# Optimization experiments

Measured on AMD Instinct MI355X. Metric: run time of the kernel, lower is better.

## Reference

```python
import jax, jax.numpy as jnp
import numpy as np

B, T, N, D = 16, 32, 1024, 64
H = 64            # gru_hidden_size
HEADS = 4
GH = 128          # gat_hidden_size (heads concatenated)
F = GH // HEADS   # per-head dim = 32
R = 128           # res_hidden_size
O = 32            # output_size


def setup_inputs() -> dict:
    key = jax.random.key(0)
    ks = jax.random.split(key, 26)
    rn = lambda k, s, sc=0.05: jax.random.normal(k, s, jnp.float32) * sc
    return {
        'sequential_inputs': jax.random.normal(ks[0], (B, T, N, D), jnp.float32),
        'adj_matrix': jax.random.randint(ks[1], (N, N), 0, 2, jnp.int32),
        'Wih0': rn(ks[2], (3 * H, D)), 'Whh0': rn(ks[3], (3 * H, H)),
        'bih0': rn(ks[4], (3 * H,)), 'bhh0': rn(ks[5], (3 * H,)),
        'Wih1': rn(ks[6], (3 * H, H)), 'Whh1': rn(ks[7], (3 * H, H)),
        'bih1': rn(ks[8], (3 * H,)), 'bhh1': rn(ks[9], (3 * H,)),
        'gatW': rn(ks[10], (H, HEADS, F)),
        'a_src': rn(ks[11], (HEADS, F)), 'a_dst': rn(ks[12], (HEADS, F)),
        'rW1': rn(ks[13], (GH, R)), 'rb1': rn(ks[14], (R,)),
        'rW2': rn(ks[15], (R, R)), 'rb2': rn(ks[16], (R,)),
        'fW': rn(ks[17], (R, O)), 'fb': rn(ks[18], (O,)),
        'ln_g': jnp.ones((O,), jnp.float32), 'ln_b': jnp.zeros((O,), jnp.float32),
        'nW1': rn(ks[19], (O, O)), 'nb1': rn(ks[20], (O,)),
        'nW2': rn(ks[21], (O, O)), 'nb2': rn(ks[22], (O,)),
    }


def gru_layer(x, Wih, Whh, bih, bhh):
    # x: [BN, T, Din] -> hidden states [BN, T, H] (PyTorch GRU cell math)
    bn = x.shape[0]
    hdim = Whh.shape[1]

    def step(h, x_t):
        gi = x_t @ Wih.T + bih
        gh = h @ Whh.T + bhh
        ir, iz, inn = jnp.split(gi, 3, axis=-1)
        hr, hz, hn = jnp.split(gh, 3, axis=-1)
        r = jax.nn.sigmoid(ir + hr)
        z = jax.nn.sigmoid(iz + hz)
        n = jnp.tanh(inn + r * hn)
        h_new = (1.0 - z) * n + z * h
        return h_new, h_new

    h0 = jnp.zeros((bn, hdim), x.dtype)
    _, hs = jax.lax.scan(step, h0, jnp.swapaxes(x, 0, 1))
    return jnp.swapaxes(hs, 0, 1)


def forward(seq, adj, Wih0, Whh0, bih0, bhh0, Wih1, Whh1, bih1, bhh1,
            gatW, a_src, a_dst, rW1, rb1, rW2, rb2, fW, fb, ln_g, ln_b,
            nW1, nb1, nW2, nb2):
    b, t, n, d = seq.shape
    # faithful to torch .view(B*N, T, D) on a [B,T,N,D] tensor: raw reshape
    x = seq.reshape(b * n, t, d)
    h1 = gru_layer(x, Wih0, Whh0, bih0, bhh0)
    h2 = gru_layer(h1, Wih1, Whh1, bih1, bhh1)
    gru_feat = h2[:, -1, :].reshape(b, n, -1)  # [B, N, H]

    # multi-head GAT, vectorized over batch (masked additive attention)
    Wh = jnp.einsum('bnd,dhf->bnhf', gru_feat, gatW)          # [B,N,HEADS,F]
    src = jnp.einsum('bnhf,hf->bnh', Wh, a_src)
    dst = jnp.einsum('bnhf,hf->bnh', Wh, a_dst)
    e = jax.nn.leaky_relu(src[:, :, None, :] + dst[:, None, :, :], 0.2)  # [B,N,N,HEADS]
    mask = (adj > 0)[None, :, :, None]
    e = jnp.where(mask, e, -1e9)
    attn = jax.nn.softmax(e, axis=2)                          # softmax over neighbors j
    gat = jnp.einsum('bijh,bjhf->bihf', attn, Wh).reshape(b, n, GH)
    gat = jax.nn.elu(gat)

    # Res-C: Linear-ReLU-Linear + identity skip, ReLU
    z = gat.reshape(b * n, GH)
    r = jax.nn.relu(z @ rW1 + rb1) @ rW2 + rb2
    res = jax.nn.relu(z + r)

    # Full-C: Linear -> LayerNorm -> tanh (dropout = identity in eval)
    y = res @ fW + fb
    mu = y.mean(-1, keepdims=True)
    var = ((y - mu) ** 2).mean(-1, keepdims=True)
    y = jnp.tanh((y - mu) * jax.lax.rsqrt(var + 1e-5) * ln_g + ln_b)

    # NN layer: Linear-ReLU-Linear
    out = (jax.nn.relu(y @ nW1 + nb1) @ nW2 + nb2).reshape(b, n, O)
    return out, attn


def reference(sequential_inputs, adj_matrix, Wih0, Whh0, bih0, bhh0, Wih1, Whh1,
              bih1, bhh1, gatW, a_src, a_dst, rW1, rb1, rW2, rb2, fW, fb,
              ln_g, ln_b, nW1, nb1, nW2, nb2):
    return forward(sequential_inputs, adj_matrix, Wih0, Whh0, bih0, bhh0,
                   Wih1, Whh1, bih1, bhh1, gatW, a_src, a_dst, rW1, rb1,
                   rW2, rb2, fW, fb, ln_g, ln_b, nW1, nb1, nW2, nb2)
```

## Files before the change

kernel.cpp:

```cpp
#include <hip/hip_runtime.h>

#define BB 16
#define TT 32
#define NN 1024
#define DD 64
#define HH 64
#define BN 16384
#define GH 128
#define RR 128
#define OO 32

#define LOG2E 1.44269504088896f

typedef __attribute__((ext_vector_type(8))) short short8;
typedef __attribute__((ext_vector_type(4))) float f32x4;
typedef __attribute__((ext_vector_type(8))) _Float16 half8;
typedef __attribute__((ext_vector_type(2))) __fp16 fp16x2;

#define MF16(A, B, C) __builtin_amdgcn_mfma_f32_16x16x32_f16((A), (B), (C), 0, 0, 0)

__device__ __forceinline__ float rcp_fast(float x) {
  return __builtin_amdgcn_rcpf(x);
}
__device__ __forceinline__ float exp2_fast(float x) {
  return __builtin_amdgcn_exp2f(x);
}
__device__ __forceinline__ float sigmoid2(float a) {
  return rcp_fast(1.0f + exp2_fast(-a));
}
__device__ __forceinline__ float tanh2(float a) {
  return fmaf(-2.0f, rcp_fast(exp2_fast(2.0f * a) + 1.0f), 1.0f);
}
__device__ __forceinline__ float tanh_e(float x) {
  return tanh2(x * LOG2E);
}
__device__ __forceinline__ float leaky02(float x) {
  return fmaxf(x, 0.2f * x);
}

__global__ __launch_bounds__(512, 4) void gru_fused_kernel(
    const float* __restrict__ x,
    const float* __restrict__ Wih0, const float* __restrict__ Whh0,
    const float* __restrict__ bih0, const float* __restrict__ bhh0,
    const float* __restrict__ Wih1, const float* __restrict__ Whh1,
    const float* __restrict__ bih1, const float* __restrict__ bhh1,
    const float* __restrict__ gatW, const float* __restrict__ a_src,
    const float* __restrict__ a_dst,
    float* __restrict__ Wh, float* __restrict__ srcv, float* __restrict__ dstv)
{
  __shared__ _Float16 sX[2][2048];
  __shared__ _Float16 sH0[2][2048];
  __shared__ _Float16 sH1[2][2048];

  const int tid = threadIdx.x;
  const int gbase = blockIdx.x * 32;

  const int w = tid >> 6, l = tid & 63;
  const int layer = w >> 2;
  const int jt = w & 3;
  const int c = l & 15;
  const int rq = l >> 4;

  const float* Wih = layer ? Wih1 : Wih0;
  const float* Whh = layer ? Whh1 : Whh0;
  const float* bihp = layer ? bih1 : bih0;
  const float* bhhp = layer ? bhh1 : bhh0;

  half8 wf[3][2][2];
#pragma unroll
  for (int g = 0; g < 3; ++g) {
    const int row = g * 64 + jt * 16 + c;
#pragma unroll
    for (int ks = 0; ks < 2; ++ks) {
      const int col = ks * 32 + (rq << 3);
      float4 i0 = *reinterpret_cast<const float4*>(Wih + row * 64 + col);
      float4 i1 = *reinterpret_cast<const float4*>(Wih + row * 64 + col + 4);
      float4 h0 = *reinterpret_cast<const float4*>(Whh + row * 64 + col);
      float4 h1 = *reinterpret_cast<const float4*>(Whh + row * 64 + col + 4);
      float wi[8] = {i0.x, i0.y, i0.z, i0.w, i1.x, i1.y, i1.z, i1.w};
      float wh[8] = {h0.x, h0.y, h0.z, h0.w, h1.x, h1.y, h1.z, h1.w};
      half8 vih, vhh;
#pragma unroll
      for (int e = 0; e < 8; ++e) {
        vih[e] = (_Float16)(wi[e] * LOG2E);
        vhh[e] = (_Float16)(wh[e] * LOG2E);
      }
      wf[g][0][ks] = vih;
      wf[g][1][ks] = vhh;
    }
  }

  const int sseq = tid >> 4;
  const int kq = (tid & 15) << 2;
  const float* xrow = x + (size_t)(gbase + sseq) * (TT * 64) + kq;
  const int sxoff = sseq * 64 + (kq ^ ((sseq & 7) << 3));

  for (int i = tid; i < 2048; i += 512) {
    sH0[0][i] = (_Float16)0.0f;
    sH1[0][i] = (_Float16)0.0f;
  }

  float4 p = *reinterpret_cast<const float4*>(xrow);
  *reinterpret_cast<fp16x2*>(&sX[0][sxoff])     = __builtin_amdgcn_cvt_pkrtz(p.x, p.y);
  *reinterpret_cast<fp16x2*>(&sX[0][sxoff + 2]) = __builtin_amdgcn_cvt_pkrtz(p.z, p.w);
  p = *reinterpret_cast<const float4*>(xrow + 64);

  const int jj = jt * 16 + c;
  const float br  = (bihp[jj]       + bhhp[jj])      * LOG2E;
  const float bz  = (bihp[64 + jj]  + bhhp[64 + jj]) * LOG2E;
  const float bni = bihp[128 + jj] * LOG2E;
  const float bnh = bhhp[128 + jj] * LOG2E;

  int ao[2][2];
#pragma unroll
  for (int mi = 0; mi < 2; ++mi)
#pragma unroll
    for (int ks = 0; ks < 2; ++ks)
      ao[mi][ks] = (mi * 16 + c) * 64 + (((ks << 5) + (rq << 3)) ^ ((c & 7) << 3));
  int hoff[2][4];
#pragma unroll
  for (int mi = 0; mi < 2; ++mi)
#pragma unroll
    for (int q = 0; q < 4; ++q) {
      const int seq = mi * 16 + (rq << 2) + q;
      hoff[mi][q] = seq * 64 + (jj ^ ((seq & 7) << 3));
    }

  float h[2][4];
#pragma unroll
  for (int mi = 0; mi < 2; ++mi)
#pragma unroll
    for (int q = 0; q < 4; ++q) h[mi][q] = 0.0f;

  for (int t = 0; t <= TT; ++t) {
    __syncthreads();
    const int cb = t & 1, nb = cb ^ 1;
    if (t + 1 < TT) {
      *reinterpret_cast<fp16x2*>(&sX[nb][sxoff])     = __builtin_amdgcn_cvt_pkrtz(p.x, p.y);
      *reinterpret_cast<fp16x2*>(&sX[nb][sxoff + 2]) = __builtin_amdgcn_cvt_pkrtz(p.z, p.w);
    }
    if (t + 2 < TT)
      p = *reinterpret_cast<const float4*>(xrow + (t + 2) * 64);

    const bool active = layer ? (t >= 1) : (t < TT);
    if (active) {
      const _Float16* xsrc = layer ? &sH0[cb][0] : &sX[cb][0];
      const _Float16* hsrc = layer ? &sH1[nb][0] : &sH0[cb][0];
      _Float16* hdst       = layer ? &sH1[cb][0] : &sH0[nb][0];

      f32x4 accr[2], accz[2], accni[2], accnh[2];
#pragma unroll
      for (int mi = 0; mi < 2; ++mi) {
        accr[mi]  = (f32x4){br, br, br, br};
        accz[mi]  = (f32x4){bz, bz, bz, bz};
        accni[mi] = (f32x4){bni, bni, bni, bni};
        accnh[mi] = (f32x4){bnh, bnh, bnh, bnh};
      }

#pragma unroll
      for (int ks = 0; ks < 2; ++ks) {
#pragma unroll
        for (int mi = 0; mi < 2; ++mi) {
          const half8 xa = *reinterpret_cast<const half8*>(xsrc + ao[mi][ks]);
          const half8 ha = *reinterpret_cast<const half8*>(hsrc + ao[mi][ks]);
          accr[mi]  = MF16(xa, wf[0][0][ks], accr[mi]);
          accr[mi]  = MF16(ha, wf[0][1][ks], accr[mi]);
          accz[mi]  = MF16(xa, wf[1][0][ks], accz[mi]);
          accz[mi]  = MF16(ha, wf[1][1][ks], accz[mi]);
          accni[mi] = MF16(xa, wf[2][0][ks], accni[mi]);
          accnh[mi] = MF16(ha, wf[2][1][ks], accnh[mi]);
        }
      }

#pragma unroll
      for (int mi = 0; mi < 2; ++mi)
#pragma unroll
        for (int q = 0; q < 4; ++q) {
          float rg = sigmoid2(accr[mi][q]);
          float zg = sigmoid2(accz[mi][q]);
          float ng = tanh2(fmaf(rg, accnh[mi][q], accni[mi][q]));
          float hv = fmaf(zg, h[mi][q] - ng, ng);
          h[mi][q] = hv;
          hdst[hoff[mi][q]] = (_Float16)hv;
        }
    }
  }

  __syncthreads();
  float* sRed = reinterpret_cast<float*>(&sX[0][0]);
  {
    const int col = (w << 4) + c;
    half8 gb[2];
#pragma unroll
    for (int ks = 0; ks < 2; ++ks)
#pragma unroll
      for (int e = 0; e < 8; ++e) {
        const int k = ks * 32 + (rq << 3) + e;
        gb[ks][e] = (_Float16)gatW[k * 128 + col];
      }
    const float as = a_src[col], ad = a_dst[col];
    f32x4 accw[2];
#pragma unroll
    for (int mi = 0; mi < 2; ++mi) {
      accw[mi] = (f32x4){0.f, 0.f, 0.f, 0.f};
#pragma unroll
      for (int ks = 0; ks < 2; ++ks) {
        const half8 fa = *reinterpret_cast<const half8*>(&sH1[0][0] + ao[mi][ks]);
        accw[mi] = MF16(fa, gb[ks], accw[mi]);
      }
    }
#pragma unroll
    for (int mi = 0; mi < 2; ++mi)
#pragma unroll
      for (int q = 0; q < 4; ++q) {
        const int seq = mi * 16 + (rq << 2) + q;
        Wh[(size_t)(gbase + seq) * 128 + col] = accw[mi][q];
        float s = accw[mi][q] * as, d = accw[mi][q] * ad;
#pragma unroll
        for (int mm = 1; mm < 16; mm <<= 1) {
          s += __shfl_xor(s, mm, 64);
          d += __shfl_xor(d, mm, 64);
        }
        if (c == 0) {
          sRed[w * 32 + seq]       = s;
          sRed[256 + w * 32 + seq] = d;
        }
      }
  }
  __syncthreads();
  if (tid < 256) {
    const int hh = tid >> 6;
    const int rem = tid & 63;
    const int sd = rem >> 5;
    const int ii = rem & 31;
    const float v = sRed[sd * 256 + (hh * 2) * 32 + ii] +
                    sRed[sd * 256 + (hh * 2 + 1) * 32 + ii];
    float* outp = sd ? dstv : srcv;
    outp[(size_t)(gbase + ii) * 4 + hh] = v;
  }
}

__global__ __launch_bounds__(256) void attn_kernel(
    const float* __restrict__ Wh, const float* __restrict__ srcp,
    const float* __restrict__ dstp, const int* __restrict__ adj,
    float* __restrict__ attn_out, float* __restrict__ gat_out)
{
  __shared__ __align__(16) float sDst[4096];
  __shared__ __align__(16) float sSrc[128];
  __shared__ __align__(16) float sIS[128];
  __shared__ unsigned int sAdjW[32][32];
  __shared__ __align__(16) _Float16 sP[2][4][32][40];
  __shared__ __align__(16) _Float16 sB[2][4][32][40];

  const int tid = threadIdx.x;
  const int bid = blockIdx.x;
  const int swzb = ((bid & 7) << 6) | (bid >> 3);
  const int b = swzb >> 5;
  const int itile = (swzb & 31) << 5;

  for (int idx = tid; idx < 4096; idx += 256)
    sDst[idx] = dstp[(size_t)b * 4096 + idx] * LOG2E;
  if (tid < 128)
    sSrc[tid] = srcp[((size_t)b * 1024 + itile) * 4 + tid] * LOG2E;

  {
    const int row = tid >> 3;
    const int w0 = (tid & 7) << 2;
    const int* arow_g = adj + (size_t)(itile + row) * 1024 + (w0 << 5);
#pragma unroll
    for (int wq = 0; wq < 4; ++wq) {
      unsigned int word = 0;
#pragma unroll
      for (int c4 = 0; c4 < 8; ++c4) {
        int4 v = *reinterpret_cast<const int4*>(arow_g + (wq << 5) + (c4 << 2));
        word |= (unsigned)((v.x != 0) ? 1 : 0) << (c4 * 4 + 0);
        word |= (unsigned)((v.y != 0) ? 1 : 0) << (c4 * 4 + 1);
        word |= (unsigned)((v.z != 0) ? 1 : 0) << (c4 * 4 + 2);
        word |= (unsigned)((v.w != 0) ? 1 : 0) << (c4 * 4 + 3);
      }
      sAdjW[row][w0 + wq] = word;
    }
  }
  __syncthreads();

  {
    const int i = tid >> 3;
    const int par = tid & 7;
    const float4 sv = *reinterpret_cast<const float4*>(&sSrc[i * 4]);
    f32x4 acc = (f32x4){0.f, 0.f, 0.f, 0.f};
    const unsigned int bit0 = 1u << par;
    for (int kw = 0; kw < 32; ++kw) {
      const unsigned int word = sAdjW[i][kw];
#pragma unroll
      for (int e = 0; e < 4; ++e) {
        const int gj = (kw << 5) + (e << 3) + par;
        const float4 dv = *reinterpret_cast<const float4*>(&sDst[gj * 4]);
        const float mf = (word & (bit0 << (e << 3))) ? 1.0f : 0.0f;
        acc[0] = fmaf(mf, exp2_fast(leaky02(sv.x + dv.x)), acc[0]);
        acc[1] = fmaf(mf, exp2_fast(leaky02(sv.y + dv.y)), acc[1]);
        acc[2] = fmaf(mf, exp2_fast(leaky02(sv.z + dv.z)), acc[2]);
        acc[3] = fmaf(mf, exp2_fast(leaky02(sv.w + dv.w)), acc[3]);
      }
    }
#pragma unroll
    for (int m = 1; m < 8; m <<= 1) {
#pragma unroll
      for (int q = 0; q < 4; ++q) acc[q] += __shfl_xor(acc[q], m, 64);
    }
    if (par == 0) {
      float4 isv;
      isv.x = acc[0] > 0.f ? rcp_fast(acc[0]) : -1.0f;
      isv.y = acc[1] > 0.f ? rcp_fast(acc[1]) : -1.0f;
      isv.z = acc[2] > 0.f ? rcp_fast(acc[2]) : -1.0f;
      isv.w = acc[3] > 0.f ? rcp_fast(acc[3]) : -1.0f;
      *reinterpret_cast<float4*>(&sIS[i * 4]) = isv;
    }
  }
  __syncthreads();

  const int il = tid >> 3;
  const int jsub = tid & 7;
  const int wv = tid >> 6;
  const int l = tid & 63;
  const int jjB = tid & 31;
  const int fcB = tid >> 5;

  const float4 sv4 = *reinterpret_cast<const float4*>(&sSrc[il * 4]);
  const float4 is4 = *reinterpret_cast<const float4*>(&sIS[il * 4]);
  f32x4* arow_out = reinterpret_cast<f32x4*>(
      attn_out + ((size_t)(b * 1024 + itile + il)) * 4096);

  f32x4 accg[2][2];
#pragma unroll
  for (int m = 0; m < 2; ++m)
#pragma unroll
    for (int n = 0; n < 2; ++n) accg[m][n] = (f32x4){0.f, 0.f, 0.f, 0.f};

  const int frow = l & 15, fchunk = l >> 4;

  for (int jt = 0; jt < 32; ++jt) {
    const int j0 = jt << 5;
    const int cur = jt & 1;
    {
      const unsigned int word = sAdjW[il][jt];
#pragma unroll
      for (int q = 0; q < 4; ++q) {
        const int j = jsub + (q << 3);
        const int gj = j0 + j;
        const float4 dv = *reinterpret_cast<const float4*>(&sDst[gj * 4]);
        const float mf = (word & (1u << j)) ? 1.0f : 0.0f;
        f32x4 a4;
        float ex;
        ex = mf * exp2_fast(leaky02(sv4.x + dv.x)); a4[0] = ex * is4.x; if (is4.x < 0.f) a4[0] = 9.765625e-4f;
        ex = mf * exp2_fast(leaky02(sv4.y + dv.y)); a4[1] = ex * is4.y; if (is4.y < 0.f) a4[1] = 9.765625e-4f;
        ex = mf * exp2_fast(leaky02(sv4.z + dv.z)); a4[2] = ex * is4.z; if (is4.z < 0.f) a4[2] = 9.765625e-4f;
        ex = mf * exp2_fast(leaky02(sv4.w + dv.w)); a4[3] = ex * is4.w; if (is4.w < 0.f) a4[3] = 9.765625e-4f;
        __builtin_nontemporal_store(a4, &arow_out[gj]);
        sP[cur][0][il][j] = (_Float16)a4[0];
        sP[cur][1][il][j] = (_Float16)a4[1];
        sP[cur][2][il][j] = (_Float16)a4[2];
        sP[cur][3][il][j] = (_Float16)a4[3];
      }
      const float* wrow = Wh + ((size_t)(b * 1024 + j0 + jjB)) * 128 + (fcB << 4);
#pragma unroll
      for (int c4 = 0; c4 < 4; ++c4) {
        float4 v = *reinterpret_cast<const float4*>(wrow + (c4 << 2));
        float vv[4] = {v.x, v.y, v.z, v.w};
#pragma unroll
        for (int e = 0; e < 4; ++e) {
          const int hf = (fcB << 4) + (c4 << 2) + e;
          sB[cur][hf >> 5][hf & 31][jjB] = (_Float16)vv[e];
        }
      }
    }
    __syncthreads();
    {
      half8 pa[2], wb[2];
#pragma unroll
      for (int m = 0; m < 2; ++m)
        pa[m] = *reinterpret_cast<const half8*>(&sP[cur][wv][m * 16 + frow][fchunk << 3]);
#pragma unroll
      for (int n = 0; n < 2; ++n)
        wb[n] = *reinterpret_cast<const half8*>(&sB[cur][wv][n * 16 + frow][fchunk << 3]);
#pragma unroll
      for (int m = 0; m < 2; ++m)
#pragma unroll
        for (int n = 0; n < 2; ++n)
          accg[m][n] = MF16(pa[m], wb[n], accg[m][n]);
    }
  }

#pragma unroll
  for (int m = 0; m < 2; ++m)
#pragma unroll
    for (int n = 0; n < 2; ++n)
#pragma unroll
      for (int q = 0; q < 4; ++q) {
        const int i = m * 16 + (l >> 4) * 4 + q;
        const int f = n * 16 + (l & 15);
        float v = accg[m][n][q];
        v = v > 0.0f ? v : (exp2_fast(v * LOG2E) - 1.0f);
        gat_out[((size_t)(b * 1024 + itile + i)) * 128 + wv * 32 + f] = v;
      }
}

__global__ __launch_bounds__(256) void mlp_kernel(
    const float* __restrict__ gat,
    const float* __restrict__ rW1, const float* __restrict__ rb1,
    const float* __restrict__ rW2, const float* __restrict__ rb2,
    const float* __restrict__ fW,  const float* __restrict__ fb,
    const float* __restrict__ ln_g, const float* __restrict__ ln_b,
    const float* __restrict__ nW1, const float* __restrict__ nb1,
    const float* __restrict__ nW2, const float* __restrict__ nb2,
    float* __restrict__ out)
{
  __shared__ __align__(16) _Float16 zA[32 * 128];
  __shared__ __align__(16) _Float16 wB[128 * 128];
  __shared__ __align__(16) _Float16 tA[32 * 128];
  __shared__ __align__(16) float    sR[32 * 128];

  const int tid = threadIdx.x;
  const int rowbase = blockIdx.x * 32;

  for (int idx = tid; idx < 1024; idx += 256) {
    const int row = idx >> 5, k4 = (idx & 31) << 2;
    float4 v = *reinterpret_cast<const float4*>(gat + (size_t)(rowbase + row) * 128 + k4);
    const int off = row * 128 + (k4 ^ ((row & 7) << 3));
    *reinterpret_cast<fp16x2*>(&zA[off])     = __builtin_amdgcn_cvt_pkrtz(v.x, v.y);
    *reinterpret_cast<fp16x2*>(&zA[off + 2]) = __builtin_amdgcn_cvt_pkrtz(v.z, v.w);
  }
  for (int idx = tid; idx < 2048; idx += 256) {
    const int n = idx & 127, kc = (idx >> 7) << 3;
    half8 hv;
#pragma unroll
    for (int e = 0; e < 8; ++e) hv[e] = (_Float16)rW1[(kc + e) * 128 + n];
    *reinterpret_cast<half8*>(&wB[n * 128 + (kc ^ ((n & 7) << 3))]) = hv;
  }
  __syncthreads();

  const int w = tid >> 6, l = tid & 63;
  const int c = l & 15, rq = l >> 4;
  const int n0 = w << 5;

  int aoz[2][4], bo[2][4];
#pragma unroll
  for (int mi = 0; mi < 2; ++mi)
#pragma unroll
    for (int ks = 0; ks < 4; ++ks)
      aoz[mi][ks] = (mi * 16 + c) * 128 + (((ks << 5) + (rq << 3)) ^ ((c & 7) << 3));
#pragma unroll
  for (int ni = 0; ni < 2; ++ni)
#pragma unroll
    for (int ks = 0; ks < 4; ++ks)
      bo[ni][ks] = (n0 + ni * 16 + c) * 128 + (((ks << 5) + (rq << 3)) ^ ((c & 7) << 3));

  {
    f32x4 acc[2][2];
#pragma unroll
    for (int ni = 0; ni < 2; ++ni) {
      const float b = rb1[n0 + ni * 16 + c];
#pragma unroll
      for (int mi = 0; mi < 2; ++mi) acc[mi][ni] = (f32x4){b, b, b, b};
    }
#pragma unroll
    for (int ks = 0; ks < 4; ++ks) {
      half8 av[2], bv[2];
#pragma unroll
      for (int mi = 0; mi < 2; ++mi) av[mi] = *reinterpret_cast<const half8*>(&zA[aoz[mi][ks]]);
#pragma unroll
      for (int ni = 0; ni < 2; ++ni) bv[ni] = *reinterpret_cast<const half8*>(&wB[bo[ni][ks]]);
#pragma unroll
      for (int mi = 0; mi < 2; ++mi)
#pragma unroll
        for (int ni = 0; ni < 2; ++ni)
          acc[mi][ni] = MF16(av[mi], bv[ni], acc[mi][ni]);
    }
#pragma unroll
    for (int mi = 0; mi < 2; ++mi)
#pragma unroll
      for (int ni = 0; ni < 2; ++ni)
#pragma unroll
        for (int q = 0; q < 4; ++q) {
          const int row = mi * 16 + (rq << 2) + q;
          const int col = n0 + ni * 16 + c;
          tA[row * 128 + (col ^ ((row & 7) << 3))] = (_Float16)fmaxf(acc[mi][ni][q], 0.0f);
        }
  }
  __syncthreads();
  for (int idx = tid; idx < 2048; idx += 256) {
    const int n = idx & 127, kc = (idx >> 7) << 3;
    half8 hv;
#pragma unroll
    for (int e = 0; e < 8; ++e) hv[e] = (_Float16)rW2[(kc + e) * 128 + n];
    *reinterpret_cast<half8*>(&wB[n * 128 + (kc ^ ((n & 7) << 3))]) = hv;
  }
  __syncthreads();
  {
    f32x4 acc[2][2];
#pragma unroll
    for (int ni = 0; ni < 2; ++ni) {
      const float b = rb2[n0 + ni * 16 + c];
#pragma unroll
      for (int mi = 0; mi < 2; ++mi) acc[mi][ni] = (f32x4){b, b, b, b};
    }
#pragma unroll
    for (int ks = 0; ks < 4; ++ks) {
      half8 av[2], bv[2];
#pragma unroll
      for (int mi = 0; mi < 2; ++mi) av[mi] = *reinterpret_cast<const half8*>(&tA[aoz[mi][ks]]);
#pragma unroll
      for (int ni = 0; ni < 2; ++ni) bv[ni] = *reinterpret_cast<const half8*>(&wB[bo[ni][ks]]);
#pragma unroll
      for (int mi = 0; mi < 2; ++mi)
#pragma unroll
        for (int ni = 0; ni < 2; ++ni)
          acc[mi][ni] = MF16(av[mi], bv[ni], acc[mi][ni]);
    }
#pragma unroll
    for (int mi = 0; mi < 2; ++mi)
#pragma unroll
      for (int ni = 0; ni < 2; ++ni)
#pragma unroll
        for (int q = 0; q < 4; ++q) {
          const int row = mi * 16 + (rq << 2) + q;
          const int col = n0 + ni * 16 + c;
          const float zz = gat[(size_t)(rowbase + row) * 128 + col];
          sR[row * 128 + col] = fmaxf(acc[mi][ni][q] + zz, 0.0f);
        }
  }
  __syncthreads();
  float* sWf = reinterpret_cast<float*>(&wB[0]);
  for (int idx = tid; idx < 4096; idx += 256) sWf[idx] = fW[idx];
  for (int idx = tid; idx < 1024; idx += 256) {
    sWf[4096 + idx] = nW1[idx];
    sWf[5120 + idx] = nW2[idx];
  }
  if (tid < 32) {
    sWf[6144 + tid] = fb[tid];
    sWf[6176 + tid] = ln_g[tid];
    sWf[6208 + tid] = ln_b[tid];
    sWf[6240 + tid] = nb1[tid];
    sWf[6272 + tid] = nb2[tid];
  }
  __syncthreads();

  float* sY  = reinterpret_cast<float*>(&zA[0]);
  float* sT2 = reinterpret_cast<float*>(&tA[0]);
  const int o = tid & 31, rr2 = tid >> 5;
  for (int g = 0; g < 4; ++g) {
    const int r = rr2 + (g << 3);
    float y = sWf[6144 + o];
#pragma unroll 8
    for (int k = 0; k < 128; ++k) y = fmaf(sR[r * 128 + k], sWf[k * 32 + o], y);
    float mu = y;
#pragma unroll
    for (int m = 16; m >= 1; m >>= 1) mu += __shfl_xor(mu, m, 32);
    mu *= (1.0f / 32.0f);
    const float d = y - mu;
    float var = d * d;
#pragma unroll
    for (int m = 16; m >= 1; m >>= 1) var += __shfl_xor(var, m, 32);
    var *= (1.0f / 32.0f);
    const float yn = d * rsqrtf(var + 1e-5f) * sWf[6176 + o] + sWf[6208 + o];
    sY[r * 32 + o] = tanh_e(yn);
  }
  __syncthreads();
  for (int g = 0; g < 4; ++g) {
    const int r = rr2 + (g << 3);
    float a = sWf[6240 + o];
#pragma unroll
    for (int k = 0; k < 32; ++k) a = fmaf(sY[r * 32 + k], sWf[4096 + k * 32 + o], a);
    sT2[r * 32 + o] = a > 0.0f ? a : 0.0f;
  }
  __syncthreads();
  for (int g = 0; g < 4; ++g) {
    const int r = rr2 + (g << 3);
    float a = sWf[6272 + o];
#pragma unroll
    for (int k = 0; k < 32; ++k) a = fmaf(sT2[r * 32 + k], sWf[5120 + k * 32 + o], a);
    out[(size_t)(rowbase + r) * 32 + o] = a;
  }
}

extern "C" void kernel_launch(void* const* d_in, const int* in_sizes, int n_in,
                              void* d_out, int out_size, void* d_ws, size_t ws_size,
                              hipStream_t stream) {
  const float* seq   = (const float*)d_in[0];
  const int*   adj   = (const int*)d_in[1];
  const float* Wih0  = (const float*)d_in[2];
  const float* Whh0  = (const float*)d_in[3];
  const float* bih0  = (const float*)d_in[4];
  const float* bhh0  = (const float*)d_in[5];
  const float* Wih1  = (const float*)d_in[6];
  const float* Whh1  = (const float*)d_in[7];
  const float* bih1  = (const float*)d_in[8];
  const float* bhh1  = (const float*)d_in[9];
  const float* gatW  = (const float*)d_in[10];
  const float* a_src = (const float*)d_in[11];
  const float* a_dst = (const float*)d_in[12];
  const float* rW1   = (const float*)d_in[13];
  const float* rb1   = (const float*)d_in[14];
  const float* rW2   = (const float*)d_in[15];
  const float* rb2   = (const float*)d_in[16];
  const float* fW    = (const float*)d_in[17];
  const float* fb    = (const float*)d_in[18];
  const float* ln_g  = (const float*)d_in[19];
  const float* ln_b  = (const float*)d_in[20];
  const float* nW1   = (const float*)d_in[21];
  const float* nb1   = (const float*)d_in[22];
  const float* nW2   = (const float*)d_in[23];
  const float* nb2   = (const float*)d_in[24];

  float* out  = (float*)d_out;
  float* attn = out + (size_t)BN * OO;

  float* ws   = (float*)d_ws;
  float* Wh   = ws;
  float* srcv = Wh + (size_t)BN * 128;
  float* dstv = srcv + (size_t)BN * 4;
  float* gat  = dstv + (size_t)BN * 4;

  gru_fused_kernel<<<512, 512, 0, stream>>>(seq, Wih0, Whh0, bih0, bhh0,
                                            Wih1, Whh1, bih1, bhh1,
                                            gatW, a_src, a_dst, Wh, srcv, dstv);
  attn_kernel<<<512, 256, 0, stream>>>(Wh, srcv, dstv, adj, attn, gat);
  mlp_kernel<<<512, 256, 0, stream>>>(gat, rW1, rb1, rW2, rb2, fW, fb,
                                      ln_g, ln_b, nW1, nb1, nW2, nb2, out);
}
```

Baseline: 184.5 us.

## Fuse MLP tail into attention kernel via shared-memory arena

Merges the residual MLP, LayerNorm and NN layers into the end of the attention kernel. Each block's 32x128 GAT tile is kept in shared memory instead of being written to global and re-read by a separate kernel. Shared memory becomes a single 64KB arena reused between the attention and MLP phases. This removes a kernel launch and the gat round-trip through global memory. The larger shared footprint may lower occupancy of the attention phase.

```diff
diff --git a/kernel.cpp b/kernel.cpp
--- a/kernel.cpp
+++ b/kernel.cpp
@@ -243,25 +243,40 @@
 __global__ __launch_bounds__(256) void attn_kernel(
     const float* __restrict__ Wh, const float* __restrict__ srcp,
     const float* __restrict__ dstp, const int* __restrict__ adj,
-    float* __restrict__ attn_out, float* __restrict__ gat_out)
+    float* __restrict__ attn_out,
+    const float* __restrict__ rW1, const float* __restrict__ rb1,
+    const float* __restrict__ rW2, const float* __restrict__ rb2,
+    const float* __restrict__ fW,  const float* __restrict__ fb,
+    const float* __restrict__ ln_g, const float* __restrict__ ln_b,
+    const float* __restrict__ nW1, const float* __restrict__ nb1,
+    const float* __restrict__ nW2, const float* __restrict__ nb2,
+    float* __restrict__ out)
 {
-  __shared__ __align__(16) float sDst[4096];
-  __shared__ __align__(16) float sSrc[128];
-  __shared__ __align__(16) float sIS[128];
-  __shared__ unsigned int sAdjW[32][32];
-  __shared__ __align__(16) _Float16 sP[2][4][32][40];
-  __shared__ __align__(16) _Float16 sB[2][4][32][40];
+  __shared__ __align__(16) char sArena[65536];
+  float* sDst = reinterpret_cast<float*>(sArena);
+  float* sSrc = reinterpret_cast<float*>(sArena + 16384);
+  float* sIS  = reinterpret_cast<float*>(sArena + 16896);
+  unsigned int* sAdjW = reinterpret_cast<unsigned int*>(sArena + 17408);
+  _Float16* sP = reinterpret_cast<_Float16*>(sArena + 21504);
+  _Float16* sBq = reinterpret_cast<_Float16*>(sArena + 41984);
+#define SP(cur, h, i, j) sP[(((cur) * 4 + (h)) * 32 + (i)) * 40 + (j)]
+#define SB(cur, h, f, j) sBq[(((cur) * 4 + (h)) * 32 + (f)) * 40 + (j)]
+  _Float16* zA = reinterpret_cast<_Float16*>(sArena);
+  _Float16* tA = reinterpret_cast<_Float16*>(sArena + 8192);
+  float*    sR = reinterpret_cast<float*>(sArena + 16384);
+  _Float16* wB = reinterpret_cast<_Float16*>(sArena + 32768);
 
   const int tid = threadIdx.x;
   const int bid = blockIdx.x;
   const int swzb = ((bid & 7) << 6) | (bid >> 3);
   const int b = swzb >> 5;
   const int itile = (swzb & 31) << 5;
+  const int growbase = b * 1024 + itile;
 
   for (int idx = tid; idx < 4096; idx += 256)
     sDst[idx] = dstp[(size_t)b * 4096 + idx] * LOG2E;
   if (tid < 128)
-    sSrc[tid] = srcp[((size_t)b * 1024 + itile) * 4 + tid] * LOG2E;
+    sSrc[tid] = srcp[((size_t)growbase) * 4 + tid] * LOG2E;
 
   {
     const int row = tid >> 3;
@@ -278,7 +293,7 @@
         word |= (unsigned)((v.z != 0) ? 1 : 0) << (c4 * 4 + 2);
         word |= (unsigned)((v.w != 0) ? 1 : 0) << (c4 * 4 + 3);
       }
-      sAdjW[row][w0 + wq] = word;
+      sAdjW[row * 32 + w0 + wq] = word;
     }
   }
   __syncthreads();
@@ -290,7 +305,7 @@
     f32x4 acc = (f32x4){0.f, 0.f, 0.f, 0.f};
     const unsigned int bit0 = 1u << par;
     for (int kw = 0; kw < 32; ++kw) {
-      const unsigned int word = sAdjW[i][kw];
+      const unsigned int word = sAdjW[i * 32 + kw];
 #pragma unroll
       for (int e = 0; e < 4; ++e) {
         const int gj = (kw << 5) + (e << 3) + par;
@@ -328,7 +343,7 @@
   const float4 sv4 = *reinterpret_cast<const float4*>(&sSrc[il * 4]);
   const float4 is4 = *reinterpret_cast<const float4*>(&sIS[il * 4]);
   f32x4* arow_out = reinterpret_cast<f32x4*>(
-      attn_out + ((size_t)(b * 1024 + itile + il)) * 4096);
+      attn_out + ((size_t)(growbase + il)) * 4096);
 
   f32x4 accg[2][2];
 #pragma unroll
@@ -342,7 +357,7 @@
     const int j0 = jt << 5;
     const int cur = jt & 1;
     {
-      const unsigned int word = sAdjW[il][jt];
+      const unsigned int word = sAdjW[il * 32 + jt];
 #pragma unroll
       for (int q = 0; q < 4; ++q) {
         const int j = jsub + (q << 3);
@@ -356,10 +371,10 @@
         ex = mf * exp2_fast(leaky02(sv4.z + dv.z)); a4[2] = ex * is4.z; if (is4.z < 0.f) a4[2] = 9.765625e-4f;
         ex = mf * exp2_fast(leaky02(sv4.w + dv.w)); a4[3] = ex * is4.w; if (is4.w < 0.f) a4[3] = 9.765625e-4f;
         __builtin_nontemporal_store(a4, &arow_out[gj]);
-        sP[cur][0][il][j] = (_Float16)a4[0];
-        sP[cur][1][il][j] = (_Float16)a4[1];
-        sP[cur][2][il][j] = (_Float16)a4[2];
-        sP[cur][3][il][j] = (_Float16)a4[3];
+        SP(cur, 0, il, j) = (_Float16)a4[0];
+        SP(cur, 1, il, j) = (_Float16)a4[1];
+        SP(cur, 2, il, j) = (_Float16)a4[2];
+        SP(cur, 3, il, j) = (_Float16)a4[3];
       }
       const float* wrow = Wh + ((size_t)(b * 1024 + j0 + jjB)) * 128 + (fcB << 4);
 #pragma unroll
@@ -369,66 +384,41 @@
 #pragma unroll
         for (int e = 0; e < 4; ++e) {
           const int hf = (fcB << 4) + (c4 << 2) + e;
-          sB[cur][hf >> 5][hf & 31][jjB] = (_Float16)vv[e];
+          SB(cur, hf >> 5, hf & 31, jjB) = (_Float16)vv[e];
         }
       }
     }
     __syncthreads();
     {
-      half8 pa[2], wb[2];
+      half8 pa[2], wb2[2];
 #pragma unroll
       for (int m = 0; m < 2; ++m)
-        pa[m] = *reinterpret_cast<const half8*>(&sP[cur][wv][m * 16 + frow][fchunk << 3]);
+        pa[m] = *reinterpret_cast<const half8*>(&SP(cur, wv, m * 16 + frow, fchunk << 3));
 #pragma unroll
       for (int n = 0; n < 2; ++n)
-        wb[n] = *reinterpret_cast<const half8*>(&sB[cur][wv][n * 16 + frow][fchunk << 3]);
+        wb2[n] = *reinterpret_cast<const half8*>(&SB(cur, wv, n * 16 + frow, fchunk << 3));
 #pragma unroll
       for (int m = 0; m < 2; ++m)
 #pragma unroll
         for (int n = 0; n < 2; ++n)
-          accg[m][n] = MF16(pa[m], wb[n], accg[m][n]);
-    }
-  }
-
+          accg[m][n] = MF16(pa[m], wb2[n], accg[m][n]);
+    }
+  }
+
+  __syncthreads();
 #pragma unroll
   for (int m = 0; m < 2; ++m)
 #pragma unroll
     for (int n = 0; n < 2; ++n)
 #pragma unroll
       for (int q = 0; q < 4; ++q) {
-        const int i = m * 16 + (l >> 4) * 4 + q;
-        const int f = n * 16 + (l & 15);
+        const int row = m * 16 + (l >> 4) * 4 + q;
+        const int col = wv * 32 + n * 16 + (l & 15);
         float v = accg[m][n][q];
         v = v > 0.0f ? v : (exp2_fast(v * LOG2E) - 1.0f);
-        gat_out[((size_t)(b * 1024 + itile + i)) * 128 + wv * 32 + f] = v;
-      }
-}
-
-__global__ __launch_bounds__(256) void mlp_kernel(
-    const float* __restrict__ gat,
-    const float* __restrict__ rW1, const float* __restrict__ rb1,
-    const float* __restrict__ rW2, const float* __restrict__ rb2,
-    const float* __restrict__ fW,  const float* __restrict__ fb,
-    const float* __restrict__ ln_g, const float* __restrict__ ln_b,
-    const float* __restrict__ nW1, const float* __restrict__ nb1,
-    const float* __restrict__ nW2, const float* __restrict__ nb2,
-    float* __restrict__ out)
-{
-  __shared__ __align__(16) _Float16 zA[32 * 128];
-  __shared__ __align__(16) _Float16 wB[128 * 128];
-  __shared__ __align__(16) _Float16 tA[32 * 128];
-  __shared__ __align__(16) float    sR[32 * 128];
-
-  const int tid = threadIdx.x;
-  const int rowbase = blockIdx.x * 32;
-
-  for (int idx = tid; idx < 1024; idx += 256) {
-    const int row = idx >> 5, k4 = (idx & 31) << 2;
-    float4 v = *reinterpret_cast<const float4*>(gat + (size_t)(rowbase + row) * 128 + k4);
-    const int off = row * 128 + (k4 ^ ((row & 7) << 3));
-    *reinterpret_cast<fp16x2*>(&zA[off])     = __builtin_amdgcn_cvt_pkrtz(v.x, v.y);
-    *reinterpret_cast<fp16x2*>(&zA[off + 2]) = __builtin_amdgcn_cvt_pkrtz(v.z, v.w);
-  }
+        sR[row * 128 + col] = v;
+        zA[row * 128 + (col ^ ((row & 7) << 3))] = (_Float16)v;
+      }
   for (int idx = tid; idx < 2048; idx += 256) {
     const int n = idx & 127, kc = (idx >> 7) << 3;
     half8 hv;
@@ -438,9 +428,8 @@
   }
   __syncthreads();
 
-  const int w = tid >> 6, l = tid & 63;
   const int c = l & 15, rq = l >> 4;
-  const int n0 = w << 5;
+  const int n0 = wv << 5;
 
   int aoz[2][4], bo[2][4];
 #pragma unroll
@@ -458,9 +447,9 @@
     f32x4 acc[2][2];
 #pragma unroll
     for (int ni = 0; ni < 2; ++ni) {
-      const float b = rb1[n0 + ni * 16 + c];
-#pragma unroll
-      for (int mi = 0; mi < 2; ++mi) acc[mi][ni] = (f32x4){b, b, b, b};
+      const float bb = rb1[n0 + ni * 16 + c];
+#pragma unroll
+      for (int mi = 0; mi < 2; ++mi) acc[mi][ni] = (f32x4){bb, bb, bb, bb};
     }
 #pragma unroll
     for (int ks = 0; ks < 4; ++ks) {
@@ -499,9 +488,9 @@
     f32x4 acc[2][2];
 #pragma unroll
     for (int ni = 0; ni < 2; ++ni) {
-      const float b = rb2[n0 + ni * 16 + c];
-#pragma unroll
-      for (int mi = 0; mi < 2; ++mi) acc[mi][ni] = (f32x4){b, b, b, b};
+      const float bb = rb2[n0 + ni * 16 + c];
+#pragma unroll
+      for (int mi = 0; mi < 2; ++mi) acc[mi][ni] = (f32x4){bb, bb, bb, bb};
     }
 #pragma unroll
     for (int ks = 0; ks < 4; ++ks) {
@@ -524,12 +513,12 @@
         for (int q = 0; q < 4; ++q) {
           const int row = mi * 16 + (rq << 2) + q;
           const int col = n0 + ni * 16 + c;
-          const float zz = gat[(size_t)(rowbase + row) * 128 + col];
+          const float zz = sR[row * 128 + col];
           sR[row * 128 + col] = fmaxf(acc[mi][ni][q] + zz, 0.0f);
         }
   }
   __syncthreads();
-  float* sWf = reinterpret_cast<float*>(&wB[0]);
+  float* sWf = reinterpret_cast<float*>(wB);
   for (int idx = tid; idx < 4096; idx += 256) sWf[idx] = fW[idx];
   for (int idx = tid; idx < 1024; idx += 256) {
     sWf[4096 + idx] = nW1[idx];
@@ -544,8 +533,8 @@
   }
   __syncthreads();
 
-  float* sY  = reinterpret_cast<float*>(&zA[0]);
-  float* sT2 = reinterpret_cast<float*>(&tA[0]);
+  float* sY  = reinterpret_cast<float*>(zA);
+  float* sT2 = reinterpret_cast<float*>(tA);
   const int o = tid & 31, rr2 = tid >> 5;
   for (int g = 0; g < 4; ++g) {
     const int r = rr2 + (g << 3);
@@ -578,8 +567,10 @@
     float a = sWf[6272 + o];
 #pragma unroll
     for (int k = 0; k < 32; ++k) a = fmaf(sT2[r * 32 + k], sWf[5120 + k * 32 + o], a);
-    out[(size_t)(rowbase + r) * 32 + o] = a;
-  }
+    out[(size_t)(growbase + r) * 32 + o] = a;
+  }
+#undef SP
+#undef SB
 }
 
 extern "C" void kernel_launch(void* const* d_in, const int* in_sizes, int n_in,
@@ -618,12 +609,11 @@
   float* Wh   = ws;
   float* srcv = Wh + (size_t)BN * 128;
   float* dstv = srcv + (size_t)BN * 4;
-  float* gat  = dstv + (size_t)BN * 4;
 
   gru_fused_kernel<<<512, 512, 0, stream>>>(seq, Wih0, Whh0, bih0, bhh0,
                                             Wih1, Whh1, bih1, bhh1,
                                             gatW, a_src, a_dst, Wh, srcv, dstv);
-  attn_kernel<<<512, 256, 0, stream>>>(Wh, srcv, dstv, adj, attn, gat);
-  mlp_kernel<<<512, 256, 0, stream>>>(gat, rW1, rb1, rW2, rb2, fW, fb,
-                                      ln_g, ln_b, nW1, nb1, nW2, nb2, out);
-}
+  attn_kernel<<<512, 256, 0, stream>>>(Wh, srcv, dstv, adj, attn,
+                                       rW1, rb1, rW2, rb2, fW, fb,
+                                       ln_g, ln_b, nW1, nb1, nW2, nb2, out);
+}
```

Result: no change. 183.1 us (-0.8%).
